# Performance work log

Hardware: AMD Instinct MI355X
Metric: run time of the kernel (lower is better)

The kernel has to match this reference:

```python
import jax, jax.numpy as jnp
import numpy as np

BATCH = 8192
IN_F = 1024
OUT_F = 1024
GRID = 5
K = 3            # spline order (degree)
SCALE = 1.0      # scale_spline


def setup_inputs() -> dict:
    key = jax.random.key(0)
    k1, k2, k3 = jax.random.split(key, 3)
    x = jax.random.normal(k1, (BATCH, IN_F), dtype=jnp.float32)
    # kaiming_uniform_(a=sqrt(5)) on (out,in) -> U(-1/sqrt(in), 1/sqrt(in))
    bound = 1.0 / np.sqrt(IN_F)
    base_weight = jax.random.uniform(k2, (OUT_F, IN_F), jnp.float32, -bound, bound)
    # normal(mean=0, std=0.1), shape (out, in, grid_size + spline_order)
    spline_weight = 0.1 * jax.random.normal(k3, (OUT_F, IN_F, GRID + K), dtype=jnp.float32)
    # extended knot vector: uniform grid on [-1,1] with spacing h, padded by K knots each side
    h = 2.0 / GRID
    knots = jnp.arange(-K, GRID + K + 1, dtype=jnp.float32) * h - 1.0  # (GRID+2K+1,)
    grid = jnp.tile(knots[None, :], (IN_F, 1))                          # (in, GRID+2K+1)
    return {"x": x, "base_weight": base_weight, "spline_weight": spline_weight, "grid": grid}


def _b_splines(x, grid, k):
    # x: (B, in), grid: (in, G+2k+1) -> basis: (B, in, G+k)
    xe = x[..., None]  # (B, in, 1)
    basis = ((xe >= grid[:, :-1]) & (xe < grid[:, 1:])).astype(x.dtype)  # degree-0, (B,in,G+2k)
    for p in range(1, k + 1):  # Cox-de Boor recursion, degree p
        left = (xe - grid[:, :-(p + 1)]) / (grid[:, p:-1] - grid[:, :-(p + 1)]) * basis[..., :-1]
        right = (grid[:, (p + 1):] - xe) / (grid[:, (p + 1):] - grid[:, 1:-p]) * basis[..., 1:]
        basis = left + right
    return basis


def reference(x, base_weight, spline_weight, grid):
    base = x @ base_weight.T                                   # (B, out)
    basis = _b_splines(x, grid, K)                             # (B, in, G+K)
    spline = jnp.einsum('bic,oic->bo', basis, spline_weight)   # (B, out)
    return base + SCALE * spline
```

## Files before the change

kernel.cpp:

```cpp
#include <hip/hip_runtime.h>


#define BATCH 8192
#define IN_F  1024
#define OUT_F 1024
#define NC    9
#define KAUG  (IN_F * NC)

typedef float  f32x4  __attribute__((ext_vector_type(4)));
typedef __bf16 bf16x8 __attribute__((ext_vector_type(8)));
typedef unsigned short u16;
typedef u16 u16x8 __attribute__((ext_vector_type(8)));

__device__ __forceinline__ u16 f2bf(float f) {
  unsigned int u = __builtin_bit_cast(unsigned int, f);
  u += 0x7FFFu + ((u >> 16) & 1u);
  return (u16)(u >> 16);
}

#define KT(j) ((float)((j) - 3) * 0.4f - 1.0f)

__device__ __forceinline__ void bspline8(float x, float bas[11]) {
#pragma unroll
  for (int j = 0; j < 11; ++j)
    bas[j] = (x >= KT(j) && x < KT(j + 1)) ? 1.0f : 0.0f;
#pragma unroll
  for (int p = 1; p <= 3; ++p) {
#pragma unroll
    for (int j = 0; j < 11 - p; ++j) {
      bas[j] = (x - KT(j)) * (1.0f / (KT(j + p) - KT(j))) * bas[j]
             + (KT(j + p + 1) - x) * (1.0f / (KT(j + p + 1) - KT(j + 1))) * bas[j + 1];
    }
  }
}

__global__ __launch_bounds__(256) void build_AW(const float* __restrict__ X,
                                                const float* __restrict__ BW,
                                                const float* __restrict__ SW,
                                                u16* __restrict__ Aa,
                                                u16* __restrict__ Wa) {
  const int idx = blockIdx.x * 256 + threadIdx.x;
  if (idx < BATCH * 128) {
    const int b  = idx >> 7;
    const int i0 = (idx & 127) << 3;
    const float4* xp = (const float4*)(X + (size_t)b * IN_F + i0);
    float4 xa = xp[0], xb = xp[1];
    float xs[8] = {xa.x, xa.y, xa.z, xa.w, xb.x, xb.y, xb.z, xb.w};
    u16x8 out[9];
#pragma unroll
    for (int e = 0; e < 8; ++e) {
      const float x = xs[e];
      out[0][e] = f2bf(x);
      float bas[11];
      bspline8(x, bas);
#pragma unroll
      for (int c = 0; c < 8; ++c) out[c + 1][e] = f2bf(bas[c]);
    }
    u16* row = Aa + (size_t)b * KAUG + i0;
#pragma unroll
    for (int c = 0; c < 9; ++c) *(u16x8*)(row + c * IN_F) = out[c];
  } else {
    const int wdx = idx - BATCH * 128;
    const int o  = wdx >> 7;
    const int i0 = (wdx & 127) << 3;
    u16x8 out[9];
    const float4* bp = (const float4*)(BW + (size_t)o * IN_F + i0);
    float4 b0 = bp[0], b1 = bp[1];
    float bs[8] = {b0.x, b0.y, b0.z, b0.w, b1.x, b1.y, b1.z, b1.w};
#pragma unroll
    for (int e = 0; e < 8; ++e) out[0][e] = f2bf(bs[e]);
    const float4* sp = (const float4*)(SW + ((size_t)o * IN_F + i0) * 8);
#pragma unroll
    for (int e = 0; e < 8; ++e) {
      float4 s0 = sp[e * 2], s1 = sp[e * 2 + 1];
      out[1][e] = f2bf(s0.x);
      out[2][e] = f2bf(s0.y);
      out[3][e] = f2bf(s0.z);
      out[4][e] = f2bf(s0.w);
      out[5][e] = f2bf(s1.x);
      out[6][e] = f2bf(s1.y);
      out[7][e] = f2bf(s1.z);
      out[8][e] = f2bf(s1.w);
    }
    u16* row = Wa + (size_t)o * KAUG + i0;
#pragma unroll
    for (int c = 0; c < 9; ++c) *(u16x8*)(row + c * IN_F) = out[c];
  }
}

#define BM 256
#define BN 128
#define BK 64
#define NT (KAUG / BK)

__device__ __forceinline__ void async16(const u16* g, u16* l) {
  __builtin_amdgcn_global_load_lds(
      (const __attribute__((address_space(1))) u16*)g,
      (__attribute__((address_space(3))) u16*)l,
      16, 0, 0);
}

__global__ __launch_bounds__(512) void gemm_bt(
    const u16* __restrict__ A,
    const u16* __restrict__ B,
    float* __restrict__ C) {
  constexpr int N = OUT_F, K = KAUG;
  __shared__ __align__(16) u16 sm[3][24576];

  const int tid = threadIdx.x;

  const int bid = blockIdx.x;
  const int wg  = (bid & 7) * 32 + (bid >> 3);
  const int bm  = wg >> 3;
  const int bn  = wg & 7;

  const int lane = tid & 63;
  const int wid  = tid >> 6;
  const int wm   = wid >> 1;
  const int wn   = wid & 1;
  const int fr   = lane & 15;
  const int hi   = lane >> 4;

  const int ak0 = ((hi      ^ (fr & 7)) << 3);
  const int ak1 = (((4 | hi) ^ (fr & 7)) << 3);
  int arow[4], brow[4];
#pragma unroll
  for (int m = 0; m < 4; ++m) arow[m] = (wm * 64 + m * 16 + fr) * 64;
#pragma unroll
  for (int n = 0; n < 4; ++n) brow[n] = 16384 + (wn * 64 + n * 16 + fr) * 64;

  const int trow = tid >> 3;
  const int gsrc = (tid & 7) ^ (trow & 7);
  const u16* Asrc = A + (size_t)(bm * BM + trow) * K + gsrc * 8;
  const u16* Bsrc = B + (size_t)(bn * BN + trow) * K + gsrc * 8;

#pragma unroll
  for (int tt = 0; tt < 2; ++tt) {
    u16* dA = &sm[tt][0] + tid * 8;
    u16* dB = &sm[tt][16384] + tid * 8;
    const size_t kg = (size_t)tt * BK;
    async16(Asrc + kg, dA);
    async16(Asrc + (size_t)64  * K + kg, dA + 4096);
    async16(Asrc + (size_t)128 * K + kg, dA + 8192);
    async16(Asrc + (size_t)192 * K + kg, dA + 12288);
    async16(Bsrc + kg, dB);
    async16(Bsrc + (size_t)64  * K + kg, dB + 4096);
  }

  f32x4 acc[4][4] = {};

  for (int t = 0; t < NT; ++t) {
    const int cur = t % 3;
    const int nxt = (t + 2) % 3;
    const bool pf = (t + 2) < NT;
    const size_t kg = (size_t)(t + 2) * BK;
    const u16* s0 = &sm[cur][0];
    u16* dA = &sm[nxt][0] + tid * 8;
    u16* dB = &sm[nxt][16384] + tid * 8;

    if (t < NT - 1) asm volatile("s_waitcnt vmcnt(6)" ::: "memory");
    else            asm volatile("s_waitcnt vmcnt(0)" ::: "memory");
    __builtin_amdgcn_s_barrier();
    __builtin_amdgcn_sched_barrier(0);

    bf16x8 bf[4], a0, a1;
#pragma unroll
    for (int n = 0; n < 4; ++n) bf[n] = *(const bf16x8*)(s0 + brow[n] + ak0);
    a0 = *(const bf16x8*)(s0 + arow[0] + ak0);
    a1 = *(const bf16x8*)(s0 + arow[1] + ak0);
    if (pf) {
      async16(Asrc + kg, dA);
      async16(Asrc + (size_t)64 * K + kg, dA + 4096);
    }
    __builtin_amdgcn_s_barrier();
    __builtin_amdgcn_s_setprio(1);
#pragma unroll
    for (int n = 0; n < 4; ++n)
      acc[0][n] = __builtin_amdgcn_mfma_f32_16x16x32_bf16(a0, bf[n], acc[0][n], 0, 0, 0);
#pragma unroll
    for (int n = 0; n < 4; ++n)
      acc[1][n] = __builtin_amdgcn_mfma_f32_16x16x32_bf16(a1, bf[n], acc[1][n], 0, 0, 0);
    __builtin_amdgcn_s_setprio(0);
    __builtin_amdgcn_s_barrier();
    a0 = *(const bf16x8*)(s0 + arow[2] + ak0);
    a1 = *(const bf16x8*)(s0 + arow[3] + ak0);
    if (pf) {
      async16(Asrc + (size_t)128 * K + kg, dA + 8192);
      async16(Asrc + (size_t)192 * K + kg, dA + 12288);
    }
    __builtin_amdgcn_s_barrier();
    __builtin_amdgcn_s_setprio(1);
#pragma unroll
    for (int n = 0; n < 4; ++n)
      acc[2][n] = __builtin_amdgcn_mfma_f32_16x16x32_bf16(a0, bf[n], acc[2][n], 0, 0, 0);
#pragma unroll
    for (int n = 0; n < 4; ++n)
      acc[3][n] = __builtin_amdgcn_mfma_f32_16x16x32_bf16(a1, bf[n], acc[3][n], 0, 0, 0);
    __builtin_amdgcn_s_setprio(0);
    __builtin_amdgcn_s_barrier();
#pragma unroll
    for (int n = 0; n < 4; ++n) bf[n] = *(const bf16x8*)(s0 + brow[n] + ak1);
    a0 = *(const bf16x8*)(s0 + arow[0] + ak1);
    a1 = *(const bf16x8*)(s0 + arow[1] + ak1);
    if (pf) {
      async16(Bsrc + kg, dB);
      async16(Bsrc + (size_t)64 * K + kg, dB + 4096);
    }
    __builtin_amdgcn_s_barrier();
    __builtin_amdgcn_s_setprio(1);
#pragma unroll
    for (int n = 0; n < 4; ++n)
      acc[0][n] = __builtin_amdgcn_mfma_f32_16x16x32_bf16(a0, bf[n], acc[0][n], 0, 0, 0);
#pragma unroll
    for (int n = 0; n < 4; ++n)
      acc[1][n] = __builtin_amdgcn_mfma_f32_16x16x32_bf16(a1, bf[n], acc[1][n], 0, 0, 0);
    __builtin_amdgcn_s_setprio(0);
    __builtin_amdgcn_s_barrier();
    a0 = *(const bf16x8*)(s0 + arow[2] + ak1);
    a1 = *(const bf16x8*)(s0 + arow[3] + ak1);
    __builtin_amdgcn_s_barrier();
    __builtin_amdgcn_s_setprio(1);
#pragma unroll
    for (int n = 0; n < 4; ++n)
      acc[2][n] = __builtin_amdgcn_mfma_f32_16x16x32_bf16(a0, bf[n], acc[2][n], 0, 0, 0);
#pragma unroll
    for (int n = 0; n < 4; ++n)
      acc[3][n] = __builtin_amdgcn_mfma_f32_16x16x32_bf16(a1, bf[n], acc[3][n], 0, 0, 0);
    __builtin_amdgcn_s_setprio(0);
    __builtin_amdgcn_s_barrier();
  }

  const int r0 = bm * BM + wm * 64 + hi * 4;
  const int c0 = bn * BN + wn * 64 + fr;
#pragma unroll
  for (int i = 0; i < 4; ++i)
#pragma unroll
    for (int j = 0; j < 4; ++j) {
      float* cp = C + (size_t)(r0 + i * 16) * N + (c0 + j * 16);
#pragma unroll
      for (int r = 0; r < 4; ++r) cp[(size_t)r * N] = acc[i][j][r];
    }
}

extern "C" void kernel_launch(void* const* d_in, const int* in_sizes, int n_in,
                              void* d_out, int out_size, void* d_ws, size_t ws_size,
                              hipStream_t stream) {
  const float* x  = (const float*)d_in[0];
  const float* bw = (const float*)d_in[1];
  const float* sw = (const float*)d_in[2];
  float* out = (float*)d_out;

  u16* Aaug = (u16*)d_ws;
  u16* Waug = Aaug + (size_t)BATCH * KAUG;

  build_AW<<<dim3((BATCH + OUT_F) * 128 / 256), 256, 0, stream>>>(x, bw, sw, Aaug, Waug);
  gemm_bt<<<dim3(BATCH / BM * (OUT_F / BN)), 512, 0, stream>>>(Aaug, Waug, out);
}
```

Before: 279.7 us.

## Merge GEMM main loop into two coarse phases with fewer barriers

Restructures the per-tile inner loop of the bf16 MFMA GEMM from four fine-grained load/compute phases into two. Each phase loads all four A fragments and four B fragments, then issues 16 MFMAs, and the async prefetches are redistributed three per phase. This halves the number of workgroup barriers per K-tile and gives larger MFMA bursts. In exchange it holds more fragment registers live and gives coarser interleaving of LDS reads with MFMA across waves.

```diff
diff --git a/kernel.cpp b/kernel.cpp
--- a/kernel.cpp
+++ b/kernel.cpp
@@ -163,71 +163,41 @@
     __builtin_amdgcn_s_barrier();
     __builtin_amdgcn_sched_barrier(0);
 
-    bf16x8 bf[4], a0, a1;
+    bf16x8 aa[4], bf[4];
 #pragma unroll
     for (int n = 0; n < 4; ++n) bf[n] = *(const bf16x8*)(s0 + brow[n] + ak0);
-    a0 = *(const bf16x8*)(s0 + arow[0] + ak0);
-    a1 = *(const bf16x8*)(s0 + arow[1] + ak0);
+#pragma unroll
+    for (int m = 0; m < 4; ++m) aa[m] = *(const bf16x8*)(s0 + arow[m] + ak0);
     if (pf) {
       async16(Asrc + kg, dA);
-      async16(Asrc + (size_t)64 * K + kg, dA + 4096);
+      async16(Asrc + (size_t)64  * K + kg, dA + 4096);
+      async16(Asrc + (size_t)128 * K + kg, dA + 8192);
     }
     __builtin_amdgcn_s_barrier();
     __builtin_amdgcn_s_setprio(1);
 #pragma unroll
-    for (int n = 0; n < 4; ++n)
-      acc[0][n] = __builtin_amdgcn_mfma_f32_16x16x32_bf16(a0, bf[n], acc[0][n], 0, 0, 0);
-#pragma unroll
-    for (int n = 0; n < 4; ++n)
-      acc[1][n] = __builtin_amdgcn_mfma_f32_16x16x32_bf16(a1, bf[n], acc[1][n], 0, 0, 0);
+    for (int m = 0; m < 4; ++m)
+#pragma unroll
+      for (int n = 0; n < 4; ++n)
+        acc[m][n] = __builtin_amdgcn_mfma_f32_16x16x32_bf16(aa[m], bf[n], acc[m][n], 0, 0, 0);
     __builtin_amdgcn_s_setprio(0);
-    __builtin_amdgcn_s_barrier();
-    a0 = *(const bf16x8*)(s0 + arow[2] + ak0);
-    a1 = *(const bf16x8*)(s0 + arow[3] + ak0);
+#pragma unroll
+    for (int n = 0; n < 4; ++n) bf[n] = *(const bf16x8*)(s0 + brow[n] + ak1);
+#pragma unroll
+    for (int m = 0; m < 4; ++m) aa[m] = *(const bf16x8*)(s0 + arow[m] + ak1);
     if (pf) {
-      async16(Asrc + (size_t)128 * K + kg, dA + 8192);
       async16(Asrc + (size_t)192 * K + kg, dA + 12288);
+      async16(Bsrc + kg, dB);
+      async16(Bsrc + (size_t)64  * K + kg, dB + 4096);
     }
     __builtin_amdgcn_s_barrier();
     __builtin_amdgcn_s_setprio(1);
 #pragma unroll
-    for (int n = 0; n < 4; ++n)
-      acc[2][n] = __builtin_amdgcn_mfma_f32_16x16x32_bf16(a0, bf[n], acc[2][n], 0, 0, 0);
-#pragma unroll
-    for (int n = 0; n < 4; ++n)
-      acc[3][n] = __builtin_amdgcn_mfma_f32_16x16x32_bf16(a1, bf[n], acc[3][n], 0, 0, 0);
+    for (int m = 0; m < 4; ++m)
+#pragma unroll
+      for (int n = 0; n < 4; ++n)
+        acc[m][n] = __builtin_amdgcn_mfma_f32_16x16x32_bf16(aa[m], bf[n], acc[m][n], 0, 0, 0);
     __builtin_amdgcn_s_setprio(0);
-    __builtin_amdgcn_s_barrier();
-#pragma unroll
-    for (int n = 0; n < 4; ++n) bf[n] = *(const bf16x8*)(s0 + brow[n] + ak1);
-    a0 = *(const bf16x8*)(s0 + arow[0] + ak1);
-    a1 = *(const bf16x8*)(s0 + arow[1] + ak1);
-    if (pf) {
-      async16(Bsrc + kg, dB);
-      async16(Bsrc + (size_t)64 * K + kg, dB + 4096);
-    }
-    __builtin_amdgcn_s_barrier();
-    __builtin_amdgcn_s_setprio(1);
-#pragma unroll
-    for (int n = 0; n < 4; ++n)
-      acc[0][n] = __builtin_amdgcn_mfma_f32_16x16x32_bf16(a0, bf[n], acc[0][n], 0, 0, 0);
-#pragma unroll
-    for (int n = 0; n < 4; ++n)
-      acc[1][n] = __builtin_amdgcn_mfma_f32_16x16x32_bf16(a1, bf[n], acc[1][n], 0, 0, 0);
-    __builtin_amdgcn_s_setprio(0);
-    __builtin_amdgcn_s_barrier();
-    a0 = *(const bf16x8*)(s0 + arow[2] + ak1);
-    a1 = *(const bf16x8*)(s0 + arow[3] + ak1);
-    __builtin_amdgcn_s_barrier();
-    __builtin_amdgcn_s_setprio(1);
-#pragma unroll
-    for (int n = 0; n < 4; ++n)
-      acc[2][n] = __builtin_amdgcn_mfma_f32_16x16x32_bf16(a0, bf[n], acc[2][n], 0, 0, 0);
-#pragma unroll
-    for (int n = 0; n < 4; ++n)
-      acc[3][n] = __builtin_amdgcn_mfma_f32_16x16x32_bf16(a1, bf[n], acc[3][n], 0, 0, 0);
-    __builtin_amdgcn_s_setprio(0);
-    __builtin_amdgcn_s_barrier();
   }
 
   const int r0 = bm * BM + wm * 64 + hi * 4;
```

New measurement: 272.1 us. -2.7%, faster.
